# Optimization experiments

Measured on AMD Instinct MI355X. Metric: run time of the kernel, lower is better.

## Reference

```python
import jax, jax.numpy as jnp
import numpy as np

# ---- config (mirrors the repo-level globals) ----
B, N = 8, 1024                 # batch, points per cloud
SHAPE_SIZE = 256               # per-point shape-code width
HEAD = 8                       # point_size + 1 - shape_size passthrough channels
SC_HID = 256                   # shape_code_encoder_hidden_dims = [256]
SC_OUT = 128                   # shape_code_encoder_output_size
E = 16                         # num_categories
INTER = HEAD + SC_OUT          # 136
ENC_DIMS = [INTER, 256, 512]   # encoder_hidden_dims
LATENT = 1024                  # latent_size
DEC_DIMS = [LATENT, 1024, 2048]
MAX_PTS, PSI = 1024, 7         # max_num_points, point_size_intermediate
DEC_OUT = (PSI + 1) * MAX_PTS  # 8192


def setup_inputs() -> dict:
    key = jax.random.key(0)
    ks = jax.random.split(key, 20)
    s = 0.02
    inp = {
        'x': jax.random.normal(ks[0], (B, HEAD + SHAPE_SIZE, N), jnp.float32),
        'cats': jax.random.randint(ks[1], (B, N), 0, E),
        # per-category shape encoders: Linear(256->256) ReLU Linear(256->128)
        'W1': jax.random.normal(ks[2], (E, SHAPE_SIZE, SC_HID), jnp.float32) * s,
        'b1': jnp.zeros((E, SC_HID), jnp.float32),
        'W2': jax.random.normal(ks[3], (E, SC_HID, SC_OUT), jnp.float32) * s,
        'b2': jnp.zeros((E, SC_OUT), jnp.float32),
        # pointwise Conv1d stack 136->256->512->1024 (weights [out,in])
        'Wc1': jax.random.normal(ks[4], (ENC_DIMS[1], ENC_DIMS[0]), jnp.float32) * s,
        'bc1': jnp.zeros((ENC_DIMS[1],), jnp.float32),
        'Wc2': jax.random.normal(ks[5], (ENC_DIMS[2], ENC_DIMS[1]), jnp.float32) * s,
        'bc2': jnp.zeros((ENC_DIMS[2],), jnp.float32),
        'Wc3': jax.random.normal(ks[6], (LATENT, ENC_DIMS[2]), jnp.float32) * s,
        'bc3': jnp.zeros((LATENT,), jnp.float32),
        # decoder MLP 1024->1024->2048->8192 (weights [in,out])
        'Wd1': jax.random.normal(ks[7], (DEC_DIMS[0], DEC_DIMS[1]), jnp.float32) * s,
        'bd1': jnp.zeros((DEC_DIMS[1],), jnp.float32),
        'Wd2': jax.random.normal(ks[8], (DEC_DIMS[1], DEC_DIMS[2]), jnp.float32) * s,
        'bd2': jnp.zeros((DEC_DIMS[2],), jnp.float32),
        'Wd3': jax.random.normal(ks[9], (DEC_DIMS[2], DEC_OUT), jnp.float32) * s,
        'bd3': jnp.zeros((DEC_OUT,), jnp.float32),
    }
    return inp


def reference(x, cats, W1, b1, W2, b2, Wc1, bc1, Wc2, bc2, Wc3, bc3,
              Wd1, bd1, Wd2, bd2, Wd3, bd3):
    # ---- encoder: category-routed per-point shape MLP ----
    sf = jnp.swapaxes(x[:, -SHAPE_SIZE:, :], 1, 2)      # [B, N, 256]
    mask = jax.nn.one_hot(cats, E, dtype=x.dtype)       # [B, N, E]
    routed = jnp.zeros((B, N, SC_OUT), x.dtype)
    for e in range(E):  # fixed small expert loop; avoids [B,N,E,hid] blowup
        h = jax.nn.relu(sf @ W1[e] + b1[e])             # [B, N, 256]
        o = h @ W2[e] + b2[e]                           # [B, N, 128]
        routed = routed + mask[..., e:e + 1] * o
    xi = jnp.concatenate([x[:, :HEAD, :], jnp.swapaxes(routed, 1, 2)], axis=1)  # [B,136,N]
    # ---- pointwise conv stack + max pool ----
    h = jax.nn.relu(jnp.einsum('oc,bcn->bon', Wc1, xi) + bc1[:, None])
    h = jax.nn.relu(jnp.einsum('oc,bcn->bon', Wc2, h) + bc2[:, None])
    h = jnp.einsum('oc,bcn->bon', Wc3, h) + bc3[:, None]  # [B, 1024, N]
    latent = jnp.max(h, axis=2)                            # [B, 1024]
    # ---- decoder MLP ----
    d = jax.nn.relu(latent @ Wd1 + bd1)
    d = jax.nn.relu(d @ Wd2 + bd2)
    out = (d @ Wd3 + bd3).reshape(B, MAX_PTS, PSI + 1)     # [B, 1024, 8]
    return out, latent
```

## Files before the change

### kernel.cpp

```cpp
#include <hip/hip_runtime.h>
#include <math.h>

#define BB 8
#define NN 1024
#define HEADC 8
#define SS 256
#define SCO 128
#define NE 16
#define C1 256
#define C2 512
#define C3 1024
#define NPTS (BB*NN)
#define XCH (HEADC+SS)
#define K1P 192
#define BK 64

typedef unsigned short ushortT;
typedef __attribute__((ext_vector_type(8))) short bf16x8;
typedef __attribute__((ext_vector_type(4))) float f32x4;

#define OB_XTB    0ull
#define OB_HB     4325376ull
#define OB_H2     0ull
#define OB_XI     8519680ull
#define OB_H1     11665408ull
#define OB_WT1    15859712ull
#define OB_WT2    15958016ull
#define OB_WT3    16220160ull
#define OB_W1T    17268736ull
#define OB_W2T    19365888ull
#define OB_PMAX   20414464ull
#define OB_LAT    20676608ull
#define OB_DPARTA 20807680ull
#define OB_DPARTB 22904832ull
#define OB_DPARTC 25001984ull
#define OB_IDX    33390592ull
#define OB_OFFS   33423360ull

__device__ __forceinline__ ushortT f2b(float f) {
  unsigned u = __float_as_uint(f);
  return (ushortT)((u + 0x7FFFu + ((u >> 16) & 1u)) >> 16);
}

#define CW_S1 (256*192)
#define CW_S2 (512*256)
#define CW_S3 (1024*512)
#define PREP_P1 2304
#define PREP_P2 5056
#define PREP_P3 7104
#define PREP_GRID 7105

__global__ __launch_bounds__(256) void k_prep_all(
    const float* __restrict__ x, ushortT* __restrict__ xTb, ushortT* __restrict__ xi,
    const float* __restrict__ Wc1, const float* __restrict__ Wc2,
    const float* __restrict__ Wc3, ushortT* __restrict__ w1c,
    ushortT* __restrict__ w2c, ushortT* __restrict__ w3c,
    const float* __restrict__ W1, const float* __restrict__ W2,
    ushortT* __restrict__ W1tb, ushortT* __restrict__ W2tb,
    const int* __restrict__ cats, int* __restrict__ idx, int* __restrict__ offs) {
  __shared__ float t[32][33];
  __shared__ int cnt[NE], base[NE + 1], cur[NE];
  int bid = blockIdx.x;
  int tid = threadIdx.x;

  if (bid < PREP_P1) {
    int bx = bid & 31, by = (bid >> 5) % 9, bz = bid / 288;
    int n0 = bx * 32, c0 = by * 32;
    int tx = tid & 31, ty = tid >> 5;
    const float* s = x + (size_t)bz * XCH * NN;
    for (int yy = ty; yy < 32; yy += 8) {
      int c = c0 + yy;
      if (c < XCH) t[yy][tx] = s[(size_t)c * NN + n0 + tx];
    }
    __syncthreads();
    for (int yy = ty; yy < 32; yy += 8) {
      int n = n0 + yy, c = c0 + tx;
      if (c < XCH) {
        ushortT v = f2b(t[tx][yy]);
        xTb[(size_t)(bz * NN + n) * XCH + c] = v;
        if (c < HEADC) xi[(size_t)(bz * NN + n) * K1P + c] = v;
      }
    }
  } else if (bid < PREP_P2) {
    int i = (bid - PREP_P1) * 256 + tid;
    if (i < CW_S1) {
      int r = i / K1P, c = i - r * K1P;
      w1c[i] = (c < 136) ? f2b(Wc1[(size_t)r * 136 + c]) : (ushortT)0;
    } else if (i < CW_S1 + CW_S2) {
      int k = i - CW_S1;
      w2c[k] = f2b(Wc2[k]);
    } else if (i < CW_S1 + CW_S2 + CW_S3) {
      int k = i - CW_S1 - CW_S2;
      w3c[k] = f2b(Wc3[k]);
    }
  } else if (bid < PREP_P3) {
    int tt = bid - PREP_P2;
    int z = tt >> 6, ry = (tt >> 3) & 7, cx = tt & 7;
    const float* s;
    ushortT* d;
    int C;
    if (z < 16) { s = W1 + (size_t)z * 65536; d = W1tb + (size_t)z * 65536; C = 256; }
    else {
      if (cx >= 4) return;
      s = W2 + (size_t)(z - 16) * 32768; d = W2tb + (size_t)(z - 16) * 32768; C = 128;
    }
    int r0 = ry * 32, c0 = cx * 32;
    int tx = tid & 31, ty = tid >> 5;
    for (int yy = ty; yy < 32; yy += 8) {
      int r = r0 + yy, c = c0 + tx;
      if (c < C) t[yy][tx] = s[(size_t)r * C + c];
    }
    __syncthreads();
    for (int yy = ty; yy < 32; yy += 8) {
      int c = c0 + yy, r = r0 + tx;
      if (c < C) d[(size_t)c * 256 + r] = f2b(t[tx][yy]);
    }
  } else {
    if (tid < NE) cnt[tid] = 0;
    __syncthreads();
    for (int p = tid; p < NPTS; p += 256) atomicAdd(&cnt[cats[p]], 1);
    __syncthreads();
    if (tid == 0) {
      int s = 0;
      for (int e = 0; e < NE; ++e) { base[e] = s; cur[e] = s; s += cnt[e]; }
      base[NE] = s;
    }
    __syncthreads();
    for (int p = tid; p < NPTS; p += 256) {
      int pos = atomicAdd(&cur[cats[p]], 1);
      idx[pos] = p;
    }
    if (tid <= NE) offs[tid] = base[tid];
  }
}

template<int MODE>
__global__ __launch_bounds__(256) void k_gemm(
    const ushortT* __restrict__ A, int lda,
    const ushortT* __restrict__ Bt, int ldb,
    const float* __restrict__ bias,
    ushortT* __restrict__ Cb, int ldc,
    float* __restrict__ pmaxOut,
    const int* __restrict__ idx, const int* __restrict__ offsp,
    int K, int relu) {
  __shared__ ushortT As[128 * BK];
  __shared__ ushortT Bs[128 * BK];
  __shared__ int pts[128];
  __shared__ float smax[2][128];
  int tid = threadIdx.x;
  int wave = tid >> 6, lane = tid & 63;
  int wm = wave >> 1, wn = wave & 1;
  int g = lane >> 4, lr = lane & 15;
  int n0 = blockIdx.x * 128;
  int m0 = 0, nr = 128, bucket0 = 0;

  if constexpr (MODE == 2 || MODE == 3) {
    int e = blockIdx.y, t = blockIdx.z;
    int s0 = offsp[e];
    int cnt = offsp[e + 1] - s0;
    int p0 = t * 128;
    if (p0 >= cnt) return;
    nr = min(128, cnt - p0);
    bucket0 = s0 + p0;
    Bt += (size_t)e * ((MODE == 2) ? 256 * 256 : 128 * 256);
    bias += e * ((MODE == 2) ? 256 : 128);
    if (tid < 128) pts[tid] = (tid < nr) ? idx[bucket0 + tid] : 0;
  } else {
    m0 = blockIdx.y * 128;
  }

  f32x4 acc[4][4];
#pragma unroll
  for (int mi = 0; mi < 4; ++mi)
#pragma unroll
    for (int nj = 0; nj < 4; ++nj) acc[mi][nj] = (f32x4)(0.f);

  int nkt = K / BK;
  for (int kt = 0; kt < nkt; ++kt) {
    int k0 = kt * BK;
    __syncthreads();
#pragma unroll
    for (int i = 0; i < 4; ++i) {
      int c = tid + i * 256;
      int row = c >> 3, slot = c & 7;
      int ss = slot ^ (row & 7);
      uint4 v;
      if constexpr (MODE == 2) {
        if (row < nr) v = *(const uint4*)(A + (size_t)pts[row] * lda + 8 + k0 + slot * 8);
        else { v.x = v.y = v.z = v.w = 0u; }
      } else if constexpr (MODE == 3) {
        if (row < nr) v = *(const uint4*)(A + (size_t)(bucket0 + row) * lda + k0 + slot * 8);
        else { v.x = v.y = v.z = v.w = 0u; }
      } else {
        v = *(const uint4*)(A + (size_t)(m0 + row) * lda + k0 + slot * 8);
      }
      *(uint4*)(As + row * BK + ss * 8) = v;
      uint4 w = *(const uint4*)(Bt + (size_t)(n0 + row) * ldb + k0 + slot * 8);
      *(uint4*)(Bs + row * BK + ss * 8) = w;
    }
    __syncthreads();
#pragma unroll
    for (int kk = 0; kk < 2; ++kk) {
      bf16x8 av[4], bv[4];
#pragma unroll
      for (int mi = 0; mi < 4; ++mi) {
        int row = wm * 64 + mi * 16 + lr;
        int slot = (kk * 4 + g) ^ (row & 7);
        av[mi] = *(const bf16x8*)(As + row * BK + slot * 8);
      }
#pragma unroll
      for (int nj = 0; nj < 4; ++nj) {
        int row = wn * 64 + nj * 16 + lr;
        int slot = (kk * 4 + g) ^ (row & 7);
        bv[nj] = *(const bf16x8*)(Bs + row * BK + slot * 8);
      }
#pragma unroll
      for (int mi = 0; mi < 4; ++mi)
#pragma unroll
        for (int nj = 0; nj < 4; ++nj)
          acc[mi][nj] = __builtin_amdgcn_mfma_f32_16x16x32_bf16(av[mi], bv[nj], acc[mi][nj], 0, 0, 0);
    }
  }

  if constexpr (MODE == 1) {
#pragma unroll
    for (int nj = 0; nj < 4; ++nj) {
      float m = -INFINITY;
#pragma unroll
      for (int mi = 0; mi < 4; ++mi)
#pragma unroll
        for (int r = 0; r < 4; ++r) m = fmaxf(m, acc[mi][nj][r]);
      m = fmaxf(m, __shfl_xor(m, 16));
      m = fmaxf(m, __shfl_xor(m, 32));
      if (lane < 16) smax[wm][wn * 64 + nj * 16 + lr] = m;
    }
    __syncthreads();
    if (tid < 128) {
      float m = fmaxf(smax[0][tid], smax[1][tid]);
      pmaxOut[(size_t)blockIdx.y * C3 + n0 + tid] = m + bias[n0 + tid];
    }
  } else {
#pragma unroll
    for (int mi = 0; mi < 4; ++mi)
#pragma unroll
      for (int nj = 0; nj < 4; ++nj)
#pragma unroll
        for (int r = 0; r < 4; ++r) {
          int lrow = wm * 64 + mi * 16 + g * 4 + r;
          int col = n0 + wn * 64 + nj * 16 + lr;
          float v = acc[mi][nj][r] + bias[col];
          if (relu) v = fmaxf(v, 0.f);
          ushortT b = f2b(v);
          if constexpr (MODE == 0) {
            Cb[(size_t)(m0 + lrow) * ldc + col] = b;
          } else if constexpr (MODE == 2) {
            if (lrow < nr) Cb[(size_t)(bucket0 + lrow) * ldc + col] = b;
          } else {
            if (lrow < nr) Cb[(size_t)pts[lrow] * ldc + 8 + col] = b;
          }
        }
  }
}

__global__ __launch_bounds__(256) void k_latmax(
    const float* __restrict__ pmax, float* __restrict__ lat, float* __restrict__ outLat) {
  int id4 = blockIdx.x * 256 + threadIdx.x;
  int b = id4 >> 8, o4 = id4 & 255;
  f32x4 m = (f32x4)(-INFINITY);
  for (int t = 0; t < 8; ++t) {
    f32x4 v = *(const f32x4*)(pmax + (size_t)((b << 3) + t) * C3 + o4 * 4);
#pragma unroll
    for (int r = 0; r < 4; ++r) m[r] = fmaxf(m[r], v[r]);
  }
  *(f32x4*)(lat + (size_t)id4 * 4) = m;
  *(f32x4*)(outLat + (size_t)id4 * 4) = m;
}

template<int MODE, int CHUNKLOG, int T, int KCIN>
__global__ __launch_bounds__(T, 1) void k_dec(
    const float* __restrict__ Asrc, const float* __restrict__ biasIn,
    const float* __restrict__ W, float* __restrict__ part, int K, int N) {
  constexpr int CHUNK = 1 << CHUNKLOG;
  __shared__ float a[8 << CHUNKLOG];
  int i0 = blockIdx.y << CHUNKLOG;
  int tid = threadIdx.x;
  for (int idx = tid; idx < (8 << CHUNKLOG); idx += T) {
    int r = idx >> CHUNKLOG, i = idx & (CHUNK - 1);
    float v;
    if constexpr (MODE == 0) {
      v = Asrc[(size_t)r * K + i0 + i];
    } else {
      v = biasIn[i0 + i];
#pragma unroll
      for (int kc = 0; kc < KCIN; ++kc)
        v += Asrc[((size_t)kc * 8 + r) * K + i0 + i];
      v = fmaxf(v, 0.f);
    }
    a[idx] = v;
  }
  __syncthreads();
  int col = (blockIdx.x * T + tid) * 4;
  f32x4 acc[8];
#pragma unroll
  for (int r = 0; r < 8; ++r) acc[r] = (f32x4)(0.f);
  const float* wp = W + (size_t)i0 * N + col;
#pragma unroll 16
  for (int k = 0; k < CHUNK; ++k) {
    f32x4 w = *(const f32x4*)(wp + (size_t)k * N);
#pragma unroll
    for (int r = 0; r < 8; ++r) acc[r] += a[(r << CHUNKLOG) + k] * w;
  }
  float* pp = part + (size_t)(blockIdx.y * 8) * N + col;
#pragma unroll
  for (int r = 0; r < 8; ++r) *(f32x4*)(pp + (size_t)r * N) = acc[r];
}

__global__ __launch_bounds__(256) void k_reduce4(
    const float* __restrict__ part, const float* __restrict__ bias,
    float* __restrict__ out, int N, int KC) {
  int o4 = blockIdx.x * 256 + threadIdx.x;
  int col4 = o4 & ((N >> 2) - 1);
  f32x4 s = ((const f32x4*)bias)[col4];
  const f32x4* p4 = (const f32x4*)part;
#pragma unroll 8
  for (int kc = 0; kc < KC; ++kc)
    s += p4[(size_t)kc * 2 * N + o4];
  ((f32x4*)out)[o4] = s;
}

extern "C" void kernel_launch(void* const* d_in, const int* in_sizes, int n_in,
                              void* d_out, int out_size, void* d_ws, size_t ws_size,
                              hipStream_t stream) {
  const float* x    = (const float*)d_in[0];
  const int*   cats = (const int*)d_in[1];
  const float* W1   = (const float*)d_in[2];
  const float* b1   = (const float*)d_in[3];
  const float* W2   = (const float*)d_in[4];
  const float* b2   = (const float*)d_in[5];
  const float* Wc1  = (const float*)d_in[6];
  const float* bc1  = (const float*)d_in[7];
  const float* Wc2  = (const float*)d_in[8];
  const float* bc2  = (const float*)d_in[9];
  const float* Wc3  = (const float*)d_in[10];
  const float* bc3  = (const float*)d_in[11];
  const float* Wd1  = (const float*)d_in[12];
  const float* bd1  = (const float*)d_in[13];
  const float* Wd2  = (const float*)d_in[14];
  const float* bd2  = (const float*)d_in[15];
  const float* Wd3  = (const float*)d_in[16];
  const float* bd3  = (const float*)d_in[17];
  float* out = (float*)d_out;

  char* wsb = (char*)d_ws;
  ushortT* xTb  = (ushortT*)(wsb + OB_XTB);
  ushortT* hB   = (ushortT*)(wsb + OB_HB);
  ushortT* h2   = (ushortT*)(wsb + OB_H2);
  ushortT* xi   = (ushortT*)(wsb + OB_XI);
  ushortT* h1   = (ushortT*)(wsb + OB_H1);
  ushortT* Wt1b = (ushortT*)(wsb + OB_WT1);
  ushortT* Wt2b = (ushortT*)(wsb + OB_WT2);
  ushortT* Wt3b = (ushortT*)(wsb + OB_WT3);
  ushortT* W1tb = (ushortT*)(wsb + OB_W1T);
  ushortT* W2tb = (ushortT*)(wsb + OB_W2T);
  float* pmax   = (float*)(wsb + OB_PMAX);
  float* lat    = (float*)(wsb + OB_LAT);
  float* dpA    = (float*)(wsb + OB_DPARTA);
  float* dpB    = (float*)(wsb + OB_DPARTB);
  float* dpC    = (float*)(wsb + OB_DPARTC);
  int*   idx    = (int*)(wsb + OB_IDX);
  int*   offs   = (int*)(wsb + OB_OFFS);

  k_prep_all<<<PREP_GRID, 256, 0, stream>>>(
      x, xTb, xi, Wc1, Wc2, Wc3, Wt1b, Wt2b, Wt3b, W1, W2, W1tb, W2tb,
      cats, idx, offs);

  k_gemm<2><<<dim3(2, NE, 8), 256, 0, stream>>>(xTb, XCH, W1tb, 256, b1, hB, 256,
                                                nullptr, idx, offs, 256, 1);
  k_gemm<3><<<dim3(1, NE, 8), 256, 0, stream>>>(hB, 256, W2tb, 256, b2, xi, K1P,
                                                nullptr, idx, offs, 256, 0);

  k_gemm<0><<<dim3(2, 64), 256, 0, stream>>>(xi, K1P, Wt1b, K1P, bc1, h1, 256,
                                             nullptr, nullptr, nullptr, K1P, 1);
  k_gemm<0><<<dim3(4, 64), 256, 0, stream>>>(h1, 256, Wt2b, 256, bc2, h2, 512,
                                             nullptr, nullptr, nullptr, 256, 1);
  k_gemm<1><<<dim3(8, 64), 256, 0, stream>>>(h2, 512, Wt3b, 512, bc3, nullptr, 0,
                                             pmax, nullptr, nullptr, 512, 0);
  k_latmax<<<8, 256, 0, stream>>>(pmax, lat, out + 65536);

  k_dec<0, 4, 64, 0><<<dim3(4, 64), 64, 0, stream>>>(lat, nullptr, Wd1, dpA, 1024, 1024);
  k_dec<1, 5, 64, 64><<<dim3(8, 32), 64, 0, stream>>>(dpA, bd1, Wd2, dpB, 1024, 2048);
  k_dec<1, 6, 256, 32><<<dim3(8, 32), 256, 0, stream>>>(dpB, bd2, Wd3, dpC, 2048, 8192);
  k_reduce4<<<64, 256, 0, stream>>>(dpC, bd3, out, 8192, 32);
  (void)in_sizes; (void)n_in; (void)out_size; (void)ws_size;
}
```

Baseline: 307.7 us.

## Split decoder partial-sum reduction into separate kernels and double-buffer weight loads

The decoder layers no longer reduce the previous layer's split-K partials inside every block's prologue. Instead, a separate reduce kernel applies bias and ReLU once into compact activation buffers. The k_dec inner loop now preloads two 16-row weight register banks and reads shared activations as float4, so global weight loads overlap with FMAs. Block shapes change as well. The cost is two extra kernel launches and more registers per thread.

Measured after the change: 270.8 us. -12.0%, faster.

```diff
diff --git a/kernel.cpp b/kernel.cpp
--- a/kernel.cpp
+++ b/kernel.cpp
@@ -31,9 +31,11 @@
 #define OB_W2T    19365888ull
 #define OB_PMAX   20414464ull
 #define OB_LAT    20676608ull
+#define OB_D1     20709376ull
+#define OB_D2     20742144ull
 #define OB_DPARTA 20807680ull
 #define OB_DPARTB 22904832ull
-#define OB_DPARTC 25001984ull
+#define OB_DPARTC 20807680ull
 #define OB_IDX    33390592ull
 #define OB_OFFS   33423360ull
 
@@ -276,40 +278,55 @@
   *(f32x4*)(outLat + (size_t)id4 * 4) = m;
 }
 
-template<int MODE, int CHUNKLOG, int T, int KCIN>
+template<int CHUNKLOG, int T>
 __global__ __launch_bounds__(T, 1) void k_dec(
-    const float* __restrict__ Asrc, const float* __restrict__ biasIn,
-    const float* __restrict__ W, float* __restrict__ part, int K, int N) {
+    const float* __restrict__ A, const float* __restrict__ W,
+    float* __restrict__ part, int K, int N) {
   constexpr int CHUNK = 1 << CHUNKLOG;
   __shared__ float a[8 << CHUNKLOG];
   int i0 = blockIdx.y << CHUNKLOG;
   int tid = threadIdx.x;
-  for (int idx = tid; idx < (8 << CHUNKLOG); idx += T) {
-    int r = idx >> CHUNKLOG, i = idx & (CHUNK - 1);
-    float v;
-    if constexpr (MODE == 0) {
-      v = Asrc[(size_t)r * K + i0 + i];
-    } else {
-      v = biasIn[i0 + i];
-#pragma unroll
-      for (int kc = 0; kc < KCIN; ++kc)
-        v += Asrc[((size_t)kc * 8 + r) * K + i0 + i];
-      v = fmaxf(v, 0.f);
-    }
-    a[idx] = v;
-  }
+  for (int idx = tid; idx < (8 << CHUNKLOG); idx += T)
+    a[idx] = A[(size_t)(idx >> CHUNKLOG) * K + i0 + (idx & (CHUNK - 1))];
   __syncthreads();
+
   int col = (blockIdx.x * T + tid) * 4;
+  const float* wp = W + (size_t)i0 * N + col;
   f32x4 acc[8];
 #pragma unroll
   for (int r = 0; r < 8; ++r) acc[r] = (f32x4)(0.f);
-  const float* wp = W + (size_t)i0 * N + col;
-#pragma unroll 16
-  for (int k = 0; k < CHUNK; ++k) {
-    f32x4 w = *(const f32x4*)(wp + (size_t)k * N);
-#pragma unroll
-    for (int r = 0; r < 8; ++r) acc[r] += a[(r << CHUNKLOG) + k] * w;
-  }
+
+  f32x4 wa[8], wb[8];
+#pragma unroll
+  for (int q = 0; q < 8; ++q) wa[q] = *(const f32x4*)(wp + (size_t)q * N);
+#pragma unroll
+  for (int q = 0; q < 8; ++q) wb[q] = *(const f32x4*)(wp + (size_t)(8 + q) * N);
+
+  for (int k0 = 0; k0 < CHUNK; k0 += 16) {
+#pragma unroll
+    for (int r = 0; r < 8; ++r) {
+      f32x4 av0 = *(const f32x4*)(&a[(r << CHUNKLOG) + k0]);
+      f32x4 av1 = *(const f32x4*)(&a[(r << CHUNKLOG) + k0 + 4]);
+      acc[r] += av0[0] * wa[0] + av0[1] * wa[1] + av0[2] * wa[2] + av0[3] * wa[3];
+      acc[r] += av1[0] * wa[4] + av1[1] * wa[5] + av1[2] * wa[6] + av1[3] * wa[7];
+    }
+    if (k0 + 16 < CHUNK) {
+#pragma unroll
+      for (int q = 0; q < 8; ++q) wa[q] = *(const f32x4*)(wp + (size_t)(k0 + 16 + q) * N);
+    }
+#pragma unroll
+    for (int r = 0; r < 8; ++r) {
+      f32x4 av0 = *(const f32x4*)(&a[(r << CHUNKLOG) + k0 + 8]);
+      f32x4 av1 = *(const f32x4*)(&a[(r << CHUNKLOG) + k0 + 12]);
+      acc[r] += av0[0] * wb[0] + av0[1] * wb[1] + av0[2] * wb[2] + av0[3] * wb[3];
+      acc[r] += av1[0] * wb[4] + av1[1] * wb[5] + av1[2] * wb[6] + av1[3] * wb[7];
+    }
+    if (k0 + 24 < CHUNK) {
+#pragma unroll
+      for (int q = 0; q < 8; ++q) wb[q] = *(const f32x4*)(wp + (size_t)(k0 + 24 + q) * N);
+    }
+  }
+
   float* pp = part + (size_t)(blockIdx.y * 8) * N + col;
 #pragma unroll
   for (int r = 0; r < 8; ++r) *(f32x4*)(pp + (size_t)r * N) = acc[r];
@@ -317,7 +334,7 @@
 
 __global__ __launch_bounds__(256) void k_reduce4(
     const float* __restrict__ part, const float* __restrict__ bias,
-    float* __restrict__ out, int N, int KC) {
+    float* __restrict__ out, int N, int KC, int doRelu) {
   int o4 = blockIdx.x * 256 + threadIdx.x;
   int col4 = o4 & ((N >> 2) - 1);
   f32x4 s = ((const f32x4*)bias)[col4];
@@ -325,6 +342,10 @@
 #pragma unroll 8
   for (int kc = 0; kc < KC; ++kc)
     s += p4[(size_t)kc * 2 * N + o4];
+  if (doRelu) {
+#pragma unroll
+    for (int r = 0; r < 4; ++r) s[r] = fmaxf(s[r], 0.f);
+  }
   ((f32x4*)out)[o4] = s;
 }
 
@@ -364,6 +385,8 @@
   ushortT* W2tb = (ushortT*)(wsb + OB_W2T);
   float* pmax   = (float*)(wsb + OB_PMAX);
   float* lat    = (float*)(wsb + OB_LAT);
+  float* d1w    = (float*)(wsb + OB_D1);
+  float* d2w    = (float*)(wsb + OB_D2);
   float* dpA    = (float*)(wsb + OB_DPARTA);
   float* dpB    = (float*)(wsb + OB_DPARTB);
   float* dpC    = (float*)(wsb + OB_DPARTC);
@@ -387,9 +410,11 @@
                                              pmax, nullptr, nullptr, 512, 0);
   k_latmax<<<8, 256, 0, stream>>>(pmax, lat, out + 65536);
 
-  k_dec<0, 4, 64, 0><<<dim3(4, 64), 64, 0, stream>>>(lat, nullptr, Wd1, dpA, 1024, 1024);
-  k_dec<1, 5, 64, 64><<<dim3(8, 32), 64, 0, stream>>>(dpA, bd1, Wd2, dpB, 1024, 2048);
-  k_dec<1, 6, 256, 32><<<dim3(8, 32), 256, 0, stream>>>(dpB, bd2, Wd3, dpC, 2048, 8192);
-  k_reduce4<<<64, 256, 0, stream>>>(dpC, bd3, out, 8192, 32);
+  k_dec<4, 128><<<dim3(2, 64), 128, 0, stream>>>(lat, Wd1, dpA, 1024, 1024);
+  k_reduce4<<<8, 256, 0, stream>>>(dpA, bd1, d1w, 1024, 64, 1);
+  k_dec<4, 128><<<dim3(4, 64), 128, 0, stream>>>(d1w, Wd2, dpB, 1024, 2048);
+  k_reduce4<<<16, 256, 0, stream>>>(dpB, bd2, d2w, 2048, 64, 1);
+  k_dec<6, 256><<<dim3(8, 32), 256, 0, stream>>>(d2w, Wd3, dpC, 2048, 8192);
+  k_reduce4<<<64, 256, 0, stream>>>(dpC, bd3, out, 8192, 32, 0);
   (void)in_sizes; (void)n_in; (void)out_size; (void)ws_size;
 }
```
